# Optimization experiments

Hardware: AMD Instinct MI355X
Metric: run time of the kernel (lower is better)

## Reference

```python
import jax, jax.numpy as jnp
import numpy as np
import itertools

N_OBJECTS = 8
NUM_VARS = 2  # num_total_variables


def _perm_indices(num_objects: int, num_vars: int):
    """Static permutation indices, matching AndLayer.build()."""
    perm_idxs = np.array(list(itertools.permutations(range(num_objects), num_vars)))  # [K, V]
    binary_idxs = np.stack(np.nonzero(1 - np.eye(num_vars))).T  # [V*(V-1), 2]
    binary_idxs = binary_idxs.reshape(num_vars, num_vars - 1, 2)
    perm_bidxs = perm_idxs[:, binary_idxs]  # [K, V, V-1, 2]
    shift = (perm_bidxs[..., 1] > perm_bidxs[..., 0]).astype(np.int64)
    perm_bidxs = np.stack([perm_bidxs[..., 0], perm_bidxs[..., 1] - shift], axis=-1)
    return perm_idxs, perm_bidxs


def setup_inputs() -> dict:
    key = jax.random.key(0)
    k0, k1, k2, k3 = jax.random.split(key, 4)
    B, N, P0, P1, P2, C = 32, N_OBJECTS, 64, 128, 64, 128
    V = NUM_VARS
    num_in = P0 + V * P1 + V * (V - 1) * P2  # 448
    return {
        "nullary_preds": jax.random.uniform(k0, (B, P0), dtype=jnp.float32),
        "unary_preds": jax.random.uniform(k1, (B, N, P1), dtype=jnp.float32),
        "binary_preds": jax.random.uniform(k2, (B, N, N - 1, P2), dtype=jnp.float32),
        "kernel": jax.random.normal(k3, (num_in, C), dtype=jnp.float32),
    }


def reference(nullary_preds, unary_preds, binary_preds, kernel):
    B = nullary_preds.shape[0]
    N = unary_preds.shape[1]
    perm_idxs, perm_bidxs = _perm_indices(N, NUM_VARS)
    K = perm_idxs.shape[0]  # number of permutations

    # [B, K, P0]
    perm_nullary = jnp.broadcast_to(nullary_preds[:, None], (B, K) + nullary_preds.shape[1:])
    # gather over object axis: [B, K, V, P1]
    perm_unary = unary_preds[:, perm_idxs]
    # gather (i, j') pairs: [B, K, V, V-1, P2]
    perm_binary = binary_preds[:, perm_bidxs[..., 0], perm_bidxs[..., 1]]

    in_tensor = jnp.concatenate(
        [perm_nullary,
         perm_unary.reshape(B, K, -1),
         perm_binary.reshape(B, K, -1)], axis=-1)  # [B, K, num_in]

    k = jnp.tanh(kernel)  # [num_in, C]
    # [B, K, num_in, C]
    weighted_truth = in_tensor[..., None] * k + (1.0 - jnp.square(k))
    conjuncts = jnp.max(jnp.min(weighted_truth, axis=2), axis=1)  # [B, C]
    return conjuncts
```

## Files before the change

kernel.cpp:

```cpp
#include <hip/hip_runtime.h>
#include <math.h>

#define BATCH   32
#define NOBJ    8
#define P0      64
#define P1      128
#define P2      64
#define COUT    128
#define KPERM   56
#define ITOT    448
#define NBGB    4
#define NIH     8
#define ISEG    (ITOT / NIH)
#define IC      8
#define NBLK    (KPERM * NBGB)
#define POISON  0xAAAAAAAAu

#define AMAX_ELEMS 4096
#define CNT_OFF    4096

__device__ __forceinline__ unsigned enc3(float f) {
    return __float_as_uint(f + 3.0f) | 0x80000000u;
}
__device__ __forceinline__ float dec3(unsigned u) {
    return __uint_as_float(u & 0x7FFFFFFFu) - 3.0f;
}
__device__ __forceinline__ float min3f(float a, float b, float c) {
    return fminf(fminf(a, b), c);
}
__device__ __forceinline__ float4 min4(float4 a, float4 b) {
    return make_float4(fminf(a.x, b.x), fminf(a.y, b.y),
                       fminf(a.z, b.z), fminf(a.w, b.w));
}
__device__ __forceinline__ float fast_tanh(float x) {
    const float e = __expf(2.0f * x);
    return fmaf(-2.0f, __builtin_amdgcn_rcpf(e + 1.0f), 1.0f);
}

__global__ __launch_bounds__(1024) void and_fused(const float* __restrict__ nullary,
                                                  const float* __restrict__ unary,
                                                  const float* __restrict__ binary,
                                                  const float* __restrict__ kern,
                                                  unsigned* __restrict__ ws,
                                                  float* __restrict__ out) {
    __shared__ float4 xs[ITOT][2];
    __shared__ float4 pm[NIH][COUT][2];
    __shared__ unsigned lastflag;

    unsigned* __restrict__ amax    = ws;
    unsigned* __restrict__ counter = ws + CNT_OFF;

    const int blk = blockIdx.x;
    const int k   = blk >> 2;
    const int bg  = blk & 3;
    const int tid = threadIdx.x;
    const int c   = tid & (COUT - 1);
    const int ih  = tid >> 7;

    const int a = k / (NOBJ - 1);
    const int r = k % (NOBJ - 1);
    const int bobj = r + (r >= a ? 1 : 0);
    const int m0 = bobj - (bobj > a ? 1 : 0);
    const int m1 = a - (a > bobj ? 1 : 0);

    float* xsf = (float*)xs;
    for (int e = tid; e < ITOT * 8; e += 1024) {
        const int i  = e >> 3;
        const int lb = e & 7;
        const int b  = bg * 8 + lb;
        float v;
        if (i < P0) {
            v = nullary[b * P0 + i];
        } else if (i < P0 + 2 * P1) {
            const int t2 = i - P0;
            const int vv = t2 >> 7;
            const int p  = t2 & (P1 - 1);
            const int n  = vv ? bobj : a;
            v = unary[(b * NOBJ + n) * P1 + p];
        } else {
            const int t2 = i - (P0 + 2 * P1);
            const int vv = t2 >> 6;
            const int p  = t2 & (P2 - 1);
            const int n  = vv ? bobj : a;
            const int m  = vv ? m1 : m0;
            v = binary[((b * NOBJ + n) * (NOBJ - 1) + m) * P2 + p];
        }
        xsf[e] = v;
    }
    __syncthreads();

    const float* __restrict__ kp = kern + c;
    float4 accL = make_float4(INFINITY, INFINITY, INFINITY, INFINITY);
    float4 accH = accL;

    const int ibase = ih * ISEG;
    for (int i0 = ibase; i0 < ibase + ISEG; i0 += IC) {
        float kv[IC];
        #pragma unroll
        for (int u = 0; u < IC; ++u) kv[u] = kp[(i0 + u) << 7];
        #pragma unroll
        for (int u = 0; u < IC; u += 2) {
            const float ta  = fast_tanh(kv[u]);
            const float tb  = fast_tanh(kv[u + 1]);
            const float bsa = fmaf(-ta, ta, 1.0f);
            const float bsb = fmaf(-tb, tb, 1.0f);
            const float4 xla = xs[i0 + u][0];
            const float4 xha = xs[i0 + u][1];
            const float4 xlb = xs[i0 + u + 1][0];
            const float4 xhb = xs[i0 + u + 1][1];
            accL.x = min3f(accL.x, fmaf(xla.x, ta, bsa), fmaf(xlb.x, tb, bsb));
            accL.y = min3f(accL.y, fmaf(xla.y, ta, bsa), fmaf(xlb.y, tb, bsb));
            accL.z = min3f(accL.z, fmaf(xla.z, ta, bsa), fmaf(xlb.z, tb, bsb));
            accL.w = min3f(accL.w, fmaf(xla.w, ta, bsa), fmaf(xlb.w, tb, bsb));
            accH.x = min3f(accH.x, fmaf(xha.x, ta, bsa), fmaf(xhb.x, tb, bsb));
            accH.y = min3f(accH.y, fmaf(xha.y, ta, bsa), fmaf(xhb.y, tb, bsb));
            accH.z = min3f(accH.z, fmaf(xha.z, ta, bsa), fmaf(xhb.z, tb, bsb));
            accH.w = min3f(accH.w, fmaf(xha.w, ta, bsa), fmaf(xhb.w, tb, bsb));
        }
    }

    pm[ih][c][0] = accL;
    pm[ih][c][1] = accH;
    __syncthreads();

    if (ih == 0) {
        float4 lo = pm[0][c][0], hi = pm[0][c][1];
        #pragma unroll
        for (int q = 1; q < NIH; ++q) {
            lo = min4(lo, pm[q][c][0]);
            hi = min4(hi, pm[q][c][1]);
        }
        unsigned* base = amax + (bg * 8) * COUT + c;
        atomicMax(base + 0 * COUT, enc3(lo.x));
        atomicMax(base + 1 * COUT, enc3(lo.y));
        atomicMax(base + 2 * COUT, enc3(lo.z));
        atomicMax(base + 3 * COUT, enc3(lo.w));
        atomicMax(base + 4 * COUT, enc3(hi.x));
        atomicMax(base + 5 * COUT, enc3(hi.y));
        atomicMax(base + 6 * COUT, enc3(hi.z));
        atomicMax(base + 7 * COUT, enc3(hi.w));
    }

    __syncthreads();
    if (tid == 0) {
        lastflag = (__hip_atomic_fetch_add(counter, 1u, __ATOMIC_RELAXED,
                                           __HIP_MEMORY_SCOPE_AGENT)
                    == POISON + (unsigned)(NBLK - 1));
    }
    __syncthreads();
    if (lastflag) {
        #pragma unroll
        for (int e = tid; e < AMAX_ELEMS; e += 1024) {
            const unsigned u =
                __hip_atomic_fetch_add(&amax[e], 0u, __ATOMIC_RELAXED,
                                       __HIP_MEMORY_SCOPE_AGENT);
            out[e] = dec3(u);
        }
    }
}

extern "C" void kernel_launch(void* const* d_in, const int* in_sizes, int n_in,
                              void* d_out, int out_size, void* d_ws, size_t ws_size,
                              hipStream_t stream) {
    const float* nullary = (const float*)d_in[0];
    const float* unary   = (const float*)d_in[1];
    const float* binary  = (const float*)d_in[2];
    const float* kern    = (const float*)d_in[3];
    float* out = (float*)d_out;

    and_fused<<<NBLK, 1024, 0, stream>>>(nullary, unary, binary, kern,
                                         (unsigned*)d_ws, out);
}
```

Baseline: 71.86 us.

## Register-tile 4 channels per thread and spread global atomics over slots

Each thread now covers 4 output channels and all 8 batch rows for a 14-input slice (32 input segments). Kernel values are loaded as float4, so each tanh is reused across 8 batches and each shared x load across 4 channels. Per-block partial minima are combined with shared-memory atomicMin on encoded values instead of a staged float4 reduction. Global atomicMax is spread over 4 slots indexed by permutation to cut contention, and the last block merges the slots. The trade-off is more registers and more shared atomics. The code also relies on the workspace slots starting out poisoned, since they are never reset.

```diff
diff --git a/kernel.cpp b/kernel.cpp
--- a/kernel.cpp
+++ b/kernel.cpp
@@ -10,14 +10,14 @@
 #define KPERM   56
 #define ITOT    448
 #define NBGB    4
-#define NIH     8
+#define NIH     32
 #define ISEG    (ITOT / NIH)
-#define IC      8
 #define NBLK    (KPERM * NBGB)
+#define NSLOT   4
+#define OUTE    (BATCH * COUT)
 #define POISON  0xAAAAAAAAu
 
-#define AMAX_ELEMS 4096
-#define CNT_OFF    4096
+#define CNT_OFF (NSLOT * OUTE)
 
 __device__ __forceinline__ unsigned enc3(float f) {
     return __float_as_uint(f + 3.0f) | 0x80000000u;
@@ -28,13 +28,28 @@
 __device__ __forceinline__ float min3f(float a, float b, float c) {
     return fminf(fminf(a, b), c);
 }
-__device__ __forceinline__ float4 min4(float4 a, float4 b) {
-    return make_float4(fminf(a.x, b.x), fminf(a.y, b.y),
-                       fminf(a.z, b.z), fminf(a.w, b.w));
-}
 __device__ __forceinline__ float fast_tanh(float x) {
     const float e = __expf(2.0f * x);
     return fmaf(-2.0f, __builtin_amdgcn_rcpf(e + 1.0f), 1.0f);
+}
+__device__ __forceinline__ float4 tanh4(float4 k) {
+    return make_float4(fast_tanh(k.x), fast_tanh(k.y),
+                       fast_tanh(k.z), fast_tanh(k.w));
+}
+__device__ __forceinline__ float4 bs4(float4 t) {
+    return make_float4(fmaf(-t.x, t.x, 1.0f), fmaf(-t.y, t.y, 1.0f),
+                       fmaf(-t.z, t.z, 1.0f), fmaf(-t.w, t.w, 1.0f));
+}
+__device__ __forceinline__ float4 fma4(float x, float4 t, float4 s) {
+    return make_float4(fmaf(x, t.x, s.x), fmaf(x, t.y, s.y),
+                       fmaf(x, t.z, s.z), fmaf(x, t.w, s.w));
+}
+__device__ __forceinline__ float4 min34(float4 a, float4 b, float4 c) {
+    return make_float4(min3f(a.x, b.x, c.x), min3f(a.y, b.y, c.y),
+                       min3f(a.z, b.z, c.z), min3f(a.w, b.w, c.w));
+}
+__device__ __forceinline__ unsigned umax2(unsigned a, unsigned b) {
+    return a > b ? a : b;
 }
 
 __global__ __launch_bounds__(1024) void and_fused(const float* __restrict__ nullary,
@@ -44,7 +59,7 @@
                                                   unsigned* __restrict__ ws,
                                                   float* __restrict__ out) {
     __shared__ float4 xs[ITOT][2];
-    __shared__ float4 pm[NIH][COUT][2];
+    __shared__ unsigned pm[NOBJ * COUT];
     __shared__ unsigned lastflag;
 
     unsigned* __restrict__ amax    = ws;
@@ -54,8 +69,8 @@
     const int k   = blk >> 2;
     const int bg  = blk & 3;
     const int tid = threadIdx.x;
-    const int c   = tid & (COUT - 1);
-    const int ih  = tid >> 7;
+    const int c4  = (tid & 31) << 2;
+    const int ih  = tid >> 5;
 
     const int a = k / (NOBJ - 1);
     const int r = k % (NOBJ - 1);
@@ -63,6 +78,7 @@
     const int m0 = bobj - (bobj > a ? 1 : 0);
     const int m1 = a - (a > bobj ? 1 : 0);
 
+    pm[tid] = 0xFFFFFFFFu;
     float* xsf = (float*)xs;
     for (int e = tid; e < ITOT * 8; e += 1024) {
         const int i  = e >> 3;
@@ -89,56 +105,51 @@
     }
     __syncthreads();
 
-    const float* __restrict__ kp = kern + c;
-    float4 accL = make_float4(INFINITY, INFINITY, INFINITY, INFINITY);
-    float4 accH = accL;
+    const float* __restrict__ kp = kern + c4;
+    float4 acc[8];
+    #pragma unroll
+    for (int b = 0; b < 8; ++b)
+        acc[b] = make_float4(INFINITY, INFINITY, INFINITY, INFINITY);
 
     const int ibase = ih * ISEG;
-    for (int i0 = ibase; i0 < ibase + ISEG; i0 += IC) {
-        float kv[IC];
-        #pragma unroll
-        for (int u = 0; u < IC; ++u) kv[u] = kp[(i0 + u) << 7];
-        #pragma unroll
-        for (int u = 0; u < IC; u += 2) {
-            const float ta  = fast_tanh(kv[u]);
-            const float tb  = fast_tanh(kv[u + 1]);
-            const float bsa = fmaf(-ta, ta, 1.0f);
-            const float bsb = fmaf(-tb, tb, 1.0f);
-            const float4 xla = xs[i0 + u][0];
-            const float4 xha = xs[i0 + u][1];
-            const float4 xlb = xs[i0 + u + 1][0];
-            const float4 xhb = xs[i0 + u + 1][1];
-            accL.x = min3f(accL.x, fmaf(xla.x, ta, bsa), fmaf(xlb.x, tb, bsb));
-            accL.y = min3f(accL.y, fmaf(xla.y, ta, bsa), fmaf(xlb.y, tb, bsb));
-            accL.z = min3f(accL.z, fmaf(xla.z, ta, bsa), fmaf(xlb.z, tb, bsb));
-            accL.w = min3f(accL.w, fmaf(xla.w, ta, bsa), fmaf(xlb.w, tb, bsb));
-            accH.x = min3f(accH.x, fmaf(xha.x, ta, bsa), fmaf(xhb.x, tb, bsb));
-            accH.y = min3f(accH.y, fmaf(xha.y, ta, bsa), fmaf(xhb.y, tb, bsb));
-            accH.z = min3f(accH.z, fmaf(xha.z, ta, bsa), fmaf(xhb.z, tb, bsb));
-            accH.w = min3f(accH.w, fmaf(xha.w, ta, bsa), fmaf(xhb.w, tb, bsb));
-        }
+    #pragma unroll
+    for (int u = 0; u < ISEG; u += 2) {
+        const int i0 = ibase + u;
+        const int i1 = i0 + 1;
+        const float4 ka = *(const float4*)(kp + (i0 << 7));
+        const float4 kb = *(const float4*)(kp + (i1 << 7));
+        const float4 ta = tanh4(ka);
+        const float4 tb = tanh4(kb);
+        const float4 sa = bs4(ta);
+        const float4 sb = bs4(tb);
+        const float4 xa0 = xs[i0][0];
+        const float4 xa1 = xs[i0][1];
+        const float4 xb0 = xs[i1][0];
+        const float4 xb1 = xs[i1][1];
+        acc[0] = min34(acc[0], fma4(xa0.x, ta, sa), fma4(xb0.x, tb, sb));
+        acc[1] = min34(acc[1], fma4(xa0.y, ta, sa), fma4(xb0.y, tb, sb));
+        acc[2] = min34(acc[2], fma4(xa0.z, ta, sa), fma4(xb0.z, tb, sb));
+        acc[3] = min34(acc[3], fma4(xa0.w, ta, sa), fma4(xb0.w, tb, sb));
+        acc[4] = min34(acc[4], fma4(xa1.x, ta, sa), fma4(xb1.x, tb, sb));
+        acc[5] = min34(acc[5], fma4(xa1.y, ta, sa), fma4(xb1.y, tb, sb));
+        acc[6] = min34(acc[6], fma4(xa1.z, ta, sa), fma4(xb1.z, tb, sb));
+        acc[7] = min34(acc[7], fma4(xa1.w, ta, sa), fma4(xb1.w, tb, sb));
     }
 
-    pm[ih][c][0] = accL;
-    pm[ih][c][1] = accH;
+    #pragma unroll
+    for (int b = 0; b < 8; ++b) {
+        atomicMin(&pm[b * COUT + c4 + 0], enc3(acc[b].x));
+        atomicMin(&pm[b * COUT + c4 + 1], enc3(acc[b].y));
+        atomicMin(&pm[b * COUT + c4 + 2], enc3(acc[b].z));
+        atomicMin(&pm[b * COUT + c4 + 3], enc3(acc[b].w));
+    }
     __syncthreads();
 
-    if (ih == 0) {
-        float4 lo = pm[0][c][0], hi = pm[0][c][1];
-        #pragma unroll
-        for (int q = 1; q < NIH; ++q) {
-            lo = min4(lo, pm[q][c][0]);
-            hi = min4(hi, pm[q][c][1]);
-        }
-        unsigned* base = amax + (bg * 8) * COUT + c;
-        atomicMax(base + 0 * COUT, enc3(lo.x));
-        atomicMax(base + 1 * COUT, enc3(lo.y));
-        atomicMax(base + 2 * COUT, enc3(lo.z));
-        atomicMax(base + 3 * COUT, enc3(lo.w));
-        atomicMax(base + 4 * COUT, enc3(hi.x));
-        atomicMax(base + 5 * COUT, enc3(hi.y));
-        atomicMax(base + 6 * COUT, enc3(hi.z));
-        atomicMax(base + 7 * COUT, enc3(hi.w));
+    {
+        const int slot = k & (NSLOT - 1);
+        const int b    = tid >> 7;
+        const int c    = tid & (COUT - 1);
+        atomicMax(amax + slot * OUTE + (bg * 8 + b) * COUT + c, pm[tid]);
     }
 
     __syncthreads();
@@ -150,11 +161,20 @@
     __syncthreads();
     if (lastflag) {
         #pragma unroll
-        for (int e = tid; e < AMAX_ELEMS; e += 1024) {
-            const unsigned u =
-                __hip_atomic_fetch_add(&amax[e], 0u, __ATOMIC_RELAXED,
+        for (int e = tid; e < OUTE; e += 1024) {
+            const unsigned u0 =
+                __hip_atomic_fetch_add(&amax[0 * OUTE + e], 0u, __ATOMIC_RELAXED,
                                        __HIP_MEMORY_SCOPE_AGENT);
-            out[e] = dec3(u);
+            const unsigned u1 =
+                __hip_atomic_fetch_add(&amax[1 * OUTE + e], 0u, __ATOMIC_RELAXED,
+                                       __HIP_MEMORY_SCOPE_AGENT);
+            const unsigned u2 =
+                __hip_atomic_fetch_add(&amax[2 * OUTE + e], 0u, __ATOMIC_RELAXED,
+                                       __HIP_MEMORY_SCOPE_AGENT);
+            const unsigned u3 =
+                __hip_atomic_fetch_add(&amax[3 * OUTE + e], 0u, __ATOMIC_RELAXED,
+                                       __HIP_MEMORY_SCOPE_AGENT);
+            out[e] = dec3(umax2(umax2(u0, u1), umax2(u2, u3)));
         }
     }
 }
```

Measured after the change: 73.86 us. 2.8% more time.

## Factor min over permutations into shared nullary/unary partial minima per batch

Applied to the files above, without the earlier changes.

Grid changes from permutation-by-batch-group blocks to batch-by-channel-group blocks. Nullary and unary partial minima are computed once per object and reused across all 56 permutations, and only the binary segment is evaluated per permutation. Tanh is precomputed once per block into LDS. Dropping the cross-block reduction removes the global atomics and the last-block counter. The cost is redundant tanh work across the 32 batch blocks and more LDS use, which may limit occupancy.

```diff
diff --git a/kernel.cpp b/kernel.cpp
--- a/kernel.cpp
+++ b/kernel.cpp
@@ -1,36 +1,21 @@
 #include <hip/hip_runtime.h>
 #include <math.h>
 
-#define BATCH   32
-#define NOBJ    8
-#define P0      64
-#define P1      128
-#define P2      64
-#define COUT    128
-#define KPERM   56
-#define ITOT    448
-#define NBGB    4
-#define NIH     8
-#define ISEG    (ITOT / NIH)
-#define IC      8
-#define NBLK    (KPERM * NBGB)
-#define POISON  0xAAAAAAAAu
+#define BATCH 32
+#define NOBJ  8
+#define P0    64
+#define P1    128
+#define P2    64
+#define COUT  128
+#define KPERM 56
+#define CG    16
+#define NBLK  (BATCH * (COUT / CG))
+#define TSR   900
+#define UST   129
+#define BST   65
 
-#define AMAX_ELEMS 4096
-#define CNT_OFF    4096
-
-__device__ __forceinline__ unsigned enc3(float f) {
-    return __float_as_uint(f + 3.0f) | 0x80000000u;
-}
-__device__ __forceinline__ float dec3(unsigned u) {
-    return __uint_as_float(u & 0x7FFFFFFFu) - 3.0f;
-}
 __device__ __forceinline__ float min3f(float a, float b, float c) {
     return fminf(fminf(a, b), c);
-}
-__device__ __forceinline__ float4 min4(float4 a, float4 b) {
-    return make_float4(fminf(a.x, b.x), fminf(a.y, b.y),
-                       fminf(a.z, b.z), fminf(a.w, b.w));
 }
 __device__ __forceinline__ float fast_tanh(float x) {
     const float e = __expf(2.0f * x);
@@ -41,122 +26,86 @@
                                                   const float* __restrict__ unary,
                                                   const float* __restrict__ binary,
                                                   const float* __restrict__ kern,
-                                                  unsigned* __restrict__ ws,
                                                   float* __restrict__ out) {
-    __shared__ float4 xs[ITOT][2];
-    __shared__ float4 pm[NIH][COUT][2];
-    __shared__ unsigned lastflag;
+    __shared__ float ts2[CG * TSR];
+    __shared__ float u_lds[NOBJ * UST];
+    __shared__ float bin_lds[KPERM * BST];
+    __shared__ float null_lds[P0];
+    __shared__ float Mt[2][NOBJ][CG];
+    __shared__ float NM[CG];
 
-    unsigned* __restrict__ amax    = ws;
-    unsigned* __restrict__ counter = ws + CNT_OFF;
+    const int tid   = threadIdx.x;
+    const int b     = blockIdx.x >> 3;
+    const int cbase = (blockIdx.x & 7) * CG;
 
-    const int blk = blockIdx.x;
-    const int k   = blk >> 2;
-    const int bg  = blk & 3;
-    const int tid = threadIdx.x;
-    const int c   = tid & (COUT - 1);
-    const int ih  = tid >> 7;
-
-    const int a = k / (NOBJ - 1);
-    const int r = k % (NOBJ - 1);
-    const int bobj = r + (r >= a ? 1 : 0);
-    const int m0 = bobj - (bobj > a ? 1 : 0);
-    const int m1 = a - (a > bobj ? 1 : 0);
-
-    float* xsf = (float*)xs;
-    for (int e = tid; e < ITOT * 8; e += 1024) {
-        const int i  = e >> 3;
-        const int lb = e & 7;
-        const int b  = bg * 8 + lb;
-        float v;
-        if (i < P0) {
-            v = nullary[b * P0 + i];
-        } else if (i < P0 + 2 * P1) {
-            const int t2 = i - P0;
-            const int vv = t2 >> 7;
-            const int p  = t2 & (P1 - 1);
-            const int n  = vv ? bobj : a;
-            v = unary[(b * NOBJ + n) * P1 + p];
+    for (int e = tid; e < 448 * CG; e += 1024) {
+        const int row = e >> 4, lc = e & 15;
+        const float kv = kern[row * COUT + cbase + lc];
+        const float t  = fast_tanh(kv);
+        *(float2*)&ts2[lc * TSR + 2 * row] = make_float2(t, fmaf(-t, t, 1.0f));
+    }
+    for (int e = tid; e < 4672; e += 1024) {
+        if (e < 3584) {
+            bin_lds[(e >> 6) * BST + (e & 63)] = binary[b * 3584 + e];
+        } else if (e < 4608) {
+            const int t2 = e - 3584;
+            u_lds[(t2 >> 7) * UST + (t2 & 127)] = unary[b * (NOBJ * P1) + t2];
         } else {
-            const int t2 = i - (P0 + 2 * P1);
-            const int vv = t2 >> 6;
-            const int p  = t2 & (P2 - 1);
-            const int n  = vv ? bobj : a;
-            const int m  = vv ? m1 : m0;
-            v = binary[((b * NOBJ + n) * (NOBJ - 1) + m) * P2 + p];
+            null_lds[e - 4608] = nullary[b * P0 + (e - 4608)];
         }
-        xsf[e] = v;
     }
     __syncthreads();
 
-    const float* __restrict__ kp = kern + c;
-    float4 accL = make_float4(INFINITY, INFINITY, INFINITY, INFINITY);
-    float4 accH = accL;
+    const int w    = tid >> 6;
+    const int lane = tid & 63;
+    const float* __restrict__ tsc = &ts2[w * TSR];
 
-    const int ibase = ih * ISEG;
-    for (int i0 = ibase; i0 < ibase + ISEG; i0 += IC) {
-        float kv[IC];
+    {
+        const int n = lane & 7, v = (lane >> 3) & 1, qa = lane >> 4;
+        const float* up = &u_lds[n * UST + qa * 32];
+        const int rb = P0 + v * P1 + qa * 32;
+        float m = INFINITY;
         #pragma unroll
-        for (int u = 0; u < IC; ++u) kv[u] = kp[(i0 + u) << 7];
+        for (int pp = 0; pp < 32; ++pp) {
+            const float2 tv = *(const float2*)&tsc[(rb + pp) * 2];
+            m = fminf(m, fmaf(up[pp], tv.x, tv.y));
+        }
+        m = fminf(m, __shfl_xor(m, 16));
+        m = fminf(m, __shfl_xor(m, 32));
+        if (lane < 16) Mt[v][n][w] = m;
+
+        const float2 tn = *(const float2*)&tsc[lane * 2];
+        float mn = fmaf(null_lds[lane], tn.x, tn.y);
         #pragma unroll
-        for (int u = 0; u < IC; u += 2) {
-            const float ta  = fast_tanh(kv[u]);
-            const float tb  = fast_tanh(kv[u + 1]);
-            const float bsa = fmaf(-ta, ta, 1.0f);
-            const float bsb = fmaf(-tb, tb, 1.0f);
-            const float4 xla = xs[i0 + u][0];
-            const float4 xha = xs[i0 + u][1];
-            const float4 xlb = xs[i0 + u + 1][0];
-            const float4 xhb = xs[i0 + u + 1][1];
-            accL.x = min3f(accL.x, fmaf(xla.x, ta, bsa), fmaf(xlb.x, tb, bsb));
-            accL.y = min3f(accL.y, fmaf(xla.y, ta, bsa), fmaf(xlb.y, tb, bsb));
-            accL.z = min3f(accL.z, fmaf(xla.z, ta, bsa), fmaf(xlb.z, tb, bsb));
-            accL.w = min3f(accL.w, fmaf(xla.w, ta, bsa), fmaf(xlb.w, tb, bsb));
-            accH.x = min3f(accH.x, fmaf(xha.x, ta, bsa), fmaf(xhb.x, tb, bsb));
-            accH.y = min3f(accH.y, fmaf(xha.y, ta, bsa), fmaf(xhb.y, tb, bsb));
-            accH.z = min3f(accH.z, fmaf(xha.z, ta, bsa), fmaf(xhb.z, tb, bsb));
-            accH.w = min3f(accH.w, fmaf(xha.w, ta, bsa), fmaf(xhb.w, tb, bsb));
-        }
+        for (int d = 1; d < 64; d <<= 1) mn = fminf(mn, __shfl_xor(mn, d));
+        if (lane == 0) NM[w] = mn;
     }
-
-    pm[ih][c][0] = accL;
-    pm[ih][c][1] = accH;
     __syncthreads();
 
-    if (ih == 0) {
-        float4 lo = pm[0][c][0], hi = pm[0][c][1];
+    float res;
+    {
+        const int kk = (lane < KPERM) ? lane : 0;
+        const int a  = kk / 7;
+        const int r  = kk - a * 7;
+        const int bo = r + (r >= a ? 1 : 0);
+        const int m0 = bo - (bo > a ? 1 : 0);
+        const int m1 = a  - (a > bo ? 1 : 0);
+        const float* bp0 = &bin_lds[(a  * 7 + m0) * BST];
+        const float* bp1 = &bin_lds[(bo * 7 + m1) * BST];
+        float ma = min3f(NM[w], Mt[0][a][w], Mt[1][bo][w]);
+        float mb = INFINITY;
         #pragma unroll
-        for (int q = 1; q < NIH; ++q) {
-            lo = min4(lo, pm[q][c][0]);
-            hi = min4(hi, pm[q][c][1]);
+        for (int p = 0; p < 64; p += 2) {
+            const float4 q0 = *(const float4*)&tsc[(320 + p) * 2];
+            const float4 q1 = *(const float4*)&tsc[(384 + p) * 2];
+            ma = min3f(ma, fmaf(bp0[p], q0.x, q0.y), fmaf(bp0[p + 1], q0.z, q0.w));
+            mb = min3f(mb, fmaf(bp1[p], q1.x, q1.y), fmaf(bp1[p + 1], q1.z, q1.w));
         }
-        unsigned* base = amax + (bg * 8) * COUT + c;
-        atomicMax(base + 0 * COUT, enc3(lo.x));
-        atomicMax(base + 1 * COUT, enc3(lo.y));
-        atomicMax(base + 2 * COUT, enc3(lo.z));
-        atomicMax(base + 3 * COUT, enc3(lo.w));
-        atomicMax(base + 4 * COUT, enc3(hi.x));
-        atomicMax(base + 5 * COUT, enc3(hi.y));
-        atomicMax(base + 6 * COUT, enc3(hi.z));
-        atomicMax(base + 7 * COUT, enc3(hi.w));
+        res = (lane < KPERM) ? fminf(ma, mb) : -INFINITY;
     }
-
-    __syncthreads();
-    if (tid == 0) {
-        lastflag = (__hip_atomic_fetch_add(counter, 1u, __ATOMIC_RELAXED,
-                                           __HIP_MEMORY_SCOPE_AGENT)
-                    == POISON + (unsigned)(NBLK - 1));
-    }
-    __syncthreads();
-    if (lastflag) {
-        #pragma unroll
-        for (int e = tid; e < AMAX_ELEMS; e += 1024) {
-            const unsigned u =
-                __hip_atomic_fetch_add(&amax[e], 0u, __ATOMIC_RELAXED,
-                                       __HIP_MEMORY_SCOPE_AGENT);
-            out[e] = dec3(u);
-        }
-    }
+    #pragma unroll
+    for (int d = 1; d < 64; d <<= 1) res = fmaxf(res, __shfl_xor(res, d));
+    if (lane == 0) out[b * COUT + cbase + w] = res;
 }
 
 extern "C" void kernel_launch(void* const* d_in, const int* in_sizes, int n_in,
@@ -167,7 +116,7 @@
     const float* binary  = (const float*)d_in[2];
     const float* kern    = (const float*)d_in[3];
     float* out = (float*)d_out;
+    (void)d_ws; (void)ws_size;
 
-    and_fused<<<NBLK, 1024, 0, stream>>>(nullary, unary, binary, kern,
-                                         (unsigned*)d_ws, out);
+    and_fused<<<NBLK, 1024, 0, stream>>>(nullary, unary, binary, kern, out);
 }
```

Result: slower. 73.60 us (+2.4%).
